# Optimization experiments

Measured on AMD Instinct MI355X. Metric: run time of the kernel, lower is better.

Reference implementation:

```python
import jax, jax.numpy as jnp
import numpy as np

NEG_POS = 3  # negpos_ratio from init
NEG_IOU = 0.4  # hard-coded in the torch forward


def corner_form(boxes):
    # (cx, cy, w, h) -> (x1, y1, x2, y2)
    cxcy, wh = boxes[:, :2], boxes[:, 2:]
    return jnp.concatenate([cxcy - wh / 2, cxcy + wh / 2], axis=-1)


def jaccard(a, b):
    # a: [O,4] corner boxes, b: [M,4] corner boxes -> IoU [O,M]
    lt = jnp.maximum(a[:, None, :2], b[None, :, :2])
    rb = jnp.minimum(a[:, None, 2:], b[None, :, 2:])
    wh = jnp.clip(rb - lt, 0.0, None)
    inter = wh[..., 0] * wh[..., 1]
    area_a = (a[:, 2] - a[:, 0]) * (a[:, 3] - a[:, 1])
    area_b = (b[:, 2] - b[:, 0]) * (b[:, 3] - b[:, 1])
    return inter / (area_a[:, None] + area_b[None, :] - inter)


def smooth_l1_sum(diff):
    ad = jnp.abs(diff)
    return jnp.where(ad < 1.0, 0.5 * diff * diff, ad - 0.5).sum()


def setup_inputs() -> dict:
    key = jax.random.key(0)
    k1, k2, k3, k4, k5, k6 = jax.random.split(key, 6)
    B, A, O = 32, 65536, 24
    loc_pred = jax.random.normal(k1, (B, A, 4), dtype=jnp.float32)
    conf_pred = jax.random.normal(k2, (B, A, 2), dtype=jnp.float32)
    # anchors in center form (cx, cy, w, h), all positive sizes
    cxcy = jax.random.uniform(k3, (A, 2), minval=0.0, maxval=1.0)
    wh = jax.random.uniform(k4, (A, 2), minval=0.02, maxval=0.3)
    anchors = jnp.concatenate([cxcy, wh], axis=-1).astype(jnp.float32)
    # GT: corner-form boxes with positive area, label column = 0 (binary head)
    xy1 = jax.random.uniform(k5, (B, O, 2), minval=0.0, maxval=0.7)
    gwh = jax.random.uniform(k6, (B, O, 2), minval=0.05, maxval=0.3)
    xy2 = jnp.clip(xy1 + gwh, 0.0, 1.0)
    labels = jnp.zeros((B, O, 1), dtype=jnp.float32)
    targets = jnp.concatenate([xy1, xy2, labels], axis=-1).astype(jnp.float32)
    return {"loc_pred": loc_pred, "conf_pred": conf_pred, "anchors": anchors,
            "targets": targets}


def reference(loc_pred, conf_pred, anchors, targets):
    B, A, _ = loc_pred.shape
    O = targets.shape[1]
    K = NEG_POS * O  # static top-k count (num_pos = O per image)
    anchors_c = jax.lax.stop_gradient(corner_form(anchors))

    def per_image(loc_p, conf_p, tgt):
        gt_boxes = tgt[:, :4]                       # [O,4]
        gt_labels = tgt[:, 4].astype(jnp.int32)     # [O]
        ov = jaccard(jax.lax.stop_gradient(gt_boxes), anchors_c)  # [O,A]
        match_idxs = jnp.argmax(ov, axis=1)         # best anchor per GT [O]
        iou = jnp.max(ov, axis=0)                   # best GT per anchor [A]
        loc_l = smooth_l1_sum(loc_p[match_idxs] - gt_boxes)
        pos = conf_p[match_idxs]                    # [O,2]
        # hard negative mining: among anchors with iou<0.4, take top K by
        # class-0 logit (descending sort + slice in the torch code)
        neg_scores = jnp.where(iou < NEG_IOU, conf_p[:, 0], -jnp.inf)
        _, neg_idx = jax.lax.top_k(neg_scores, K)
        neg = conf_p[neg_idx]                       # [K,2]
        logits = jnp.concatenate([pos, neg], axis=0)       # [O+K,2]
        labels = jnp.concatenate([gt_labels + 1,
                                  jnp.zeros((K,), jnp.int32)])
        ls = jax.nn.log_softmax(logits, axis=-1)
        ce = -ls[jnp.arange(O + K), labels].mean()
        return loc_l, ce

    loc_l, ce = jax.vmap(per_image)(loc_pred, conf_pred, targets)
    N = B * O  # sum of len(target) over batch
    return loc_l.sum() / N, ce.sum() / N
```

## Files before the change

### kernel.cpp

```cpp
#include <hip/hip_runtime.h>
#include <hip/hip_bf16.h>
#include <math.h>

typedef unsigned long long ull;

#define MAXO 24

__device__ __forceinline__ unsigned int xform(float x){
  unsigned int b = __float_as_uint(x);
  return (b & 0x80000000u) ? ~b : (b | 0x80000000u);
}
__device__ __forceinline__ float softplus_(float d){
  return (d > 20.f) ? d : log1pf(expf(d));
}

template<int O>
__global__ __launch_bounds__(256) void kA_t(const float4* __restrict__ anchors,
        const float* __restrict__ targets, const float2* __restrict__ conf,
        ull* __restrict__ matchbest, ull* __restrict__ negmask,
        unsigned int* __restrict__ gh1, int A){
  const int b = blockIdx.y, t = threadIdx.x, lane = t & 63;
  __shared__ ull wk[O][32];
  __shared__ unsigned int hist[2048];
  for (int i = t; i < 2048; i += 256) hist[i] = 0;
  __syncthreads();
  const float* tg = targets + (size_t)b * O * 5;
  const int base = blockIdx.x * 1024 + t;

  float ax1[4], ay1[4], ax2[4], ay2[4], aar[4], amax[4];
#pragma unroll
  for (int k = 0; k < 4; k++){
    float4 an = anchors[base + k*256];
    float hw = __fmul_rn(an.z, 0.5f), hh = __fmul_rn(an.w, 0.5f);
    ax1[k] = __fsub_rn(an.x, hw); ay1[k] = __fsub_rn(an.y, hh);
    ax2[k] = __fadd_rn(an.x, hw); ay2[k] = __fadd_rn(an.y, hh);
    aar[k] = __fmul_rn(__fsub_rn(ax2[k],ax1[k]), __fsub_rn(ay2[k],ay1[k]));
    amax[k] = 0.f;
  }

  unsigned int biou[O], bidx[O];
#pragma unroll
  for (int o = 0; o < O; o++){
    float gx1 = tg[o*5+0], gy1 = tg[o*5+1], gx2 = tg[o*5+2], gy2 = tg[o*5+3];
    float ga  = __fmul_rn(__fsub_rn(gx2,gx1), __fsub_rn(gy2,gy1));
    unsigned int bu = 0u, bi = 0u;
#pragma unroll
    for (int k = 0; k < 4; k++){
      float ltx = fmaxf(gx1, ax1[k]), lty = fmaxf(gy1, ay1[k]);
      float rbx = fminf(gx2, ax2[k]), rby = fminf(gy2, ay2[k]);
      float wx = fmaxf(__fsub_rn(rbx,ltx), 0.f);
      float wy = fmaxf(__fsub_rn(rby,lty), 0.f);
      float inter = __fmul_rn(wx, wy);
      float denom = __fsub_rn(__fadd_rn(ga, aar[k]), inter);
      float iou = __fmul_rn(inter, __builtin_amdgcn_rcpf(denom));
      amax[k] = fmaxf(amax[k], iou);
      unsigned int ub = __float_as_uint(iou);
      bool better = ub > bu;
      bi = better ? (unsigned int)(base + k*256) : bi;
      bu = better ? ub : bu;
    }
    biou[o] = bu; bidx[o] = bi;
  }

#pragma unroll
  for (int k = 0; k < 4; k++){
    bool neg = amax[k] < 0.4f;
    ull m = __ballot(neg);
    if (lane == 0) negmask[(size_t)b*(A>>6) + ((unsigned)(base + k*256) >> 6)] = m;
    if (neg){
      float cx = conf[(size_t)b*A + (unsigned)(base + k*256)].x;
      atomicAdd(&hist[xform(cx) >> 21], 1u);
    }
  }

#pragma unroll
  for (int o = 0; o < O; o++){
    ull key = ((ull)biou[o] << 32) | (unsigned int)(~bidx[o]);
#pragma unroll
    for (int s = 4; s >= 1; s >>= 1){
      ull other = (ull)__shfl_down((long long)key, (unsigned)s, 8);
      if (other > key) key = other;
    }
    if ((lane & 7) == 0) wk[o][t >> 3] = key;
  }
  __syncthreads();
  if (t < O * 8){
    int o = t >> 3, part = t & 7;
    ull k = wk[o][part*4];
#pragma unroll
    for (int j = 1; j < 4; j++){ ull v = wk[o][part*4 + j]; if (v > k) k = v; }
#pragma unroll
    for (int s = 4; s >= 1; s >>= 1){
      ull other = (ull)__shfl_down((long long)k, (unsigned)s, 8);
      if (other > k) k = other;
    }
    if (part == 0) atomicMax(&matchbest[b*O + o], k);
  }
  for (int i = t; i < 2048; i += 256){
    unsigned int v = hist[i];
    if (v) atomicAdd(&gh1[b*2048 + i], v);
  }
}

__global__ __launch_bounds__(256) void kA_g(const float4* __restrict__ anchors,
        const float* __restrict__ targets,
        ull* __restrict__ matchbest, ull* __restrict__ negmask, int A, int O){
  int b = blockIdx.y, t = threadIdx.x, lane = t & 63, wid = t >> 6;
  __shared__ float sgt[MAXO*5];
  __shared__ float sarea[MAXO];
  __shared__ ull wk[4][MAXO];
  int n5 = O*5;
  if (t < n5) sgt[t] = targets[b*n5 + t];
  __syncthreads();
  if (t < O){
    float x1=sgt[t*5], y1=sgt[t*5+1], x2=sgt[t*5+2], y2=sgt[t*5+3];
    sarea[t] = __fmul_rn(__fsub_rn(x2,x1), __fsub_rn(y2,y1));
  }
  __syncthreads();
  ull key[MAXO];
  for (int o=0;o<O;o++) key[o]=0;
  int base = blockIdx.x * 1024;
  for (int k=0;k<4;k++){
    int a = base + k*256 + t;
    float4 an = anchors[a];
    float hw = __fmul_rn(an.z, 0.5f), hh = __fmul_rn(an.w, 0.5f);
    float ax1 = __fsub_rn(an.x, hw), ay1 = __fsub_rn(an.y, hh);
    float ax2 = __fadd_rn(an.x, hw), ay2 = __fadd_rn(an.y, hh);
    float aarea = __fmul_rn(__fsub_rn(ax2,ax1), __fsub_rn(ay2,ay1));
    float amax = 0.f;
    for (int o=0;o<O;o++){
      float ltx = fmaxf(sgt[o*5+0], ax1), lty = fmaxf(sgt[o*5+1], ay1);
      float rbx = fminf(sgt[o*5+2], ax2), rby = fminf(sgt[o*5+3], ay2);
      float wx = fmaxf(__fsub_rn(rbx,ltx), 0.f);
      float wy = fmaxf(__fsub_rn(rby,lty), 0.f);
      float inter = __fmul_rn(wx, wy);
      float denom = __fsub_rn(__fadd_rn(sarea[o], aarea), inter);
      float iou = __fdiv_rn(inter, denom);
      amax = fmaxf(amax, iou);
      ull kk = ((ull)__float_as_uint(iou) << 32) | (unsigned int)(~(unsigned int)a);
      if (kk > key[o]) key[o] = kk;
    }
    ull m = __ballot(amax < 0.4f);
    if (lane == 0) negmask[(size_t)b*(A>>6) + (a>>6)] = m;
  }
  for (int o=0;o<O;o++){
    ull k = key[o];
    for (int s=32; s>=1; s>>=1){
      unsigned int lo = __shfl_down((unsigned int)(k & 0xFFFFFFFFu), s);
      unsigned int hi = __shfl_down((unsigned int)(k >> 32), s);
      ull other = ((ull)hi<<32) | lo;
      if (other > k) k = other;
    }
    if (lane == 0) wk[wid][o] = k;
  }
  __syncthreads();
  if (t < O){
    ull k = wk[0][t];
    for (int w=1; w<4; w++){ ull v = wk[w][t]; if (v>k) k=v; }
    atomicMax(&matchbest[b*O + t], k);
  }
}

__global__ __launch_bounds__(256) void kH1(const float2* __restrict__ conf,
     const ull* __restrict__ negmask, unsigned int* __restrict__ gh1, int A){
  int b = blockIdx.x, seg = blockIdx.y, t = threadIdx.x, lane = t & 63;
  __shared__ unsigned int h[2048];
  for (int i = t; i < 2048; i += 256) h[i] = 0;
  __syncthreads();
  const float2* cb = conf + (size_t)b * A;
  const ull* mb = negmask + (size_t)b * (A >> 6);
  int base = seg * 8192;
  for (int j = 0; j < 32; j++){
    int a = base + j*256 + t;
    ull w = mb[a >> 6];
    if ((w >> lane) & 1ull){
      unsigned int u = xform(cb[a].x);
      atomicAdd(&h[u >> 21], 1u);
    }
  }
  __syncthreads();
  for (int i = t; i < 2048; i += 256){
    unsigned int v = h[i];
    if (v) atomicAdd(&gh1[b*2048 + i], v);
  }
}

__global__ __launch_bounds__(1024) void kM2(const float2* __restrict__ conf,
     const ull* __restrict__ negmask, const unsigned int* __restrict__ gh1,
     const ull* __restrict__ matchbest, const float* __restrict__ loc,
     const float* __restrict__ targets, float* __restrict__ out,
     int A, int O, int K, float lscale, float cscale){
  const int b = blockIdx.x, t = threadIdx.x, lane = t & 63, wid = t >> 6;
  __shared__ unsigned int s0[2048], s1[2048];
  __shared__ ull stash[2048];
  __shared__ ull sb[256];
  __shared__ unsigned int s_cnt, s_cnt2, s_b1, s_R, s_b2, s_R2;
  __shared__ float wsum[16];

  if (t < O){
    int i = b*O + t;
    ull key = matchbest[i];
    unsigned int idx = ~(unsigned int)(key & 0xFFFFFFFFull);
    const float* tg = targets + (size_t)i*5;
    const float* lp = loc + ((size_t)b*A + idx)*4;
    float ll = 0.f;
#pragma unroll
    for (int d=0; d<4; d++){
      float df = lp[d] - tg[d];
      float ad = fabsf(df);
      ll += (ad < 1.f) ? 0.5f*df*df : (ad - 0.5f);
    }
    float2 c = conf[(size_t)b*A + idx];
    float m = fmaxf(c.x, c.y);
    float lse = m + logf(expf(c.x - m) + expf(c.y - m));
    atomicAdd(&out[0], ll * lscale);
    atomicAdd(&out[1], (lse - c.y) * cscale);
  }
  if (t == 0){ s_cnt = 0; s_cnt2 = 0; }
  for (int i = t; i < 2048; i += 1024) s0[i] = gh1[b*2048 + i];
  __syncthreads();

  {
    unsigned int* src = s0; unsigned int* dst = s1;
    for (int d = 1; d < 2048; d <<= 1){
      for (int i = t; i < 2048; i += 1024){
        unsigned int v = src[i];
        if (i + d < 2048) v += src[i + d];
        dst[i] = v;
      }
      __syncthreads();
      unsigned int* tmp = src; src = dst; dst = tmp;
    }
    for (int i = t; i < 2048; i += 1024){
      unsigned int si = src[i];
      unsigned int sn = (i < 2047) ? src[i+1] : 0u;
      if (si >= (unsigned int)K && sn < (unsigned int)K){ s_b1 = (unsigned int)i; s_R = (unsigned int)K - sn; }
    }
  }
  __syncthreads();
  const unsigned int b1 = s_b1, R = s_R;
  for (int i = t; i < 2048; i += 1024) s0[i] = 0;
  __syncthreads();

  float ce = 0.f;
  const float2* cb = conf + (size_t)b * A;
  const ull* mb = negmask + (size_t)b * (A >> 6);
  const int iters = A >> 10;
  for (int j = 0; j < iters; j++){
    int a = (j << 10) + t;
    ull w = mb[a >> 6];
    if ((w >> (a & 63)) & 1ull){
      float2 c = cb[a];
      unsigned int u = xform(c.x);
      unsigned int bin = u >> 21;
      if (bin > b1){
        ce += softplus_(c.y - c.x);
      } else if (bin == b1){
        atomicAdd(&s0[(u >> 10) & 2047u], 1u);
        unsigned int p = atomicAdd(&s_cnt, 1u);
        if (p < 2048u) stash[p] = ((ull)u << 32) | (unsigned int)(~(unsigned int)a);
      }
    }
  }
  __syncthreads();

  {
    unsigned int* src = s0; unsigned int* dst = s1;
    for (int d = 1; d < 2048; d <<= 1){
      for (int i = t; i < 2048; i += 1024){
        unsigned int v = src[i];
        if (i + d < 2048) v += src[i + d];
        dst[i] = v;
      }
      __syncthreads();
      unsigned int* tmp = src; src = dst; dst = tmp;
    }
    for (int i = t; i < 2048; i += 1024){
      unsigned int si = src[i];
      unsigned int sn = (i < 2047) ? src[i+1] : 0u;
      if (si >= R && sn < R){ s_b2 = (unsigned int)i; s_R2 = R - sn; }
    }
  }
  __syncthreads();
  const unsigned int b2 = s_b2, R2 = s_R2;
  const unsigned int cnt = (s_cnt < 2048u) ? s_cnt : 2048u;
  const bool ovf = (s_cnt > 2048u);

  if (!ovf){
    for (unsigned int i = t; i < cnt; i += 1024){
      ull e = stash[i];
      unsigned int u = (unsigned int)(e >> 32);
      unsigned int sub = (u >> 10) & 2047u;
      if (sub > b2){
        unsigned int a = ~(unsigned int)(e & 0xFFFFFFFFull);
        float2 c = cb[a];
        ce += softplus_(c.y - c.x);
      } else if (sub == b2){
        unsigned int p = atomicAdd(&s_cnt2, 1u);
        if (p < 256u) sb[p] = e;
      }
    }
  } else {
    for (int j = 0; j < iters; j++){
      int a = (j << 10) + t;
      ull w = mb[a >> 6];
      if ((w >> (a & 63)) & 1ull){
        float2 c = cb[a];
        unsigned int u = xform(c.x);
        if ((u >> 21) == b1){
          unsigned int sub = (u >> 10) & 2047u;
          if (sub > b2){
            ce += softplus_(c.y - c.x);
          } else if (sub == b2){
            unsigned int p = atomicAdd(&s_cnt2, 1u);
            if (p < 256u) sb[p] = ((ull)u << 32) | (unsigned int)(~(unsigned int)a);
          }
        }
      }
    }
  }
  __syncthreads();

  const unsigned int cnt2 = (s_cnt2 < 256u) ? s_cnt2 : 256u;
  for (unsigned int i = t; i < cnt2; i += 1024){
    ull ki = sb[i];
    unsigned int rank = 0;
    for (unsigned int j = 0; j < cnt2; j++) rank += (sb[j] > ki) ? 1u : 0u;
    if (rank < R2){
      unsigned int a = ~(unsigned int)(ki & 0xFFFFFFFFull);
      float2 c = cb[a];
      ce += softplus_(c.y - c.x);
    }
  }

#pragma unroll
  for (int s = 32; s >= 1; s >>= 1) ce += __shfl_down(ce, s);
  if (lane == 0) wsum[wid] = ce;
  __syncthreads();
  if (t == 0){
    float tot = 0.f;
    for (int w2 = 0; w2 < 16; w2++) tot += wsum[w2];
    atomicAdd(&out[1], tot * cscale);
  }
}

extern "C" void kernel_launch(void* const* d_in, const int* in_sizes, int n_in,
                              void* d_out, int out_size, void* d_ws, size_t ws_size,
                              hipStream_t stream) {
  const float*  loc     = (const float*)d_in[0];
  const float2* conf    = (const float2*)d_in[1];
  const float4* anchors = (const float4*)d_in[2];
  const float*  targets = (const float*)d_in[3];
  int A = in_sizes[2] / 4;
  int B = in_sizes[0] / (A * 4);
  int O = in_sizes[3] / (B * 5);
  int K = 3 * O;
  float* out = (float*)d_out;

  char* wsb = (char*)d_ws;
  size_t off = 0;
  ull* matchbest = (ull*)(wsb + off);              off += (size_t)B * O * sizeof(ull);
  unsigned int* gh1 = (unsigned int*)(wsb + off);  off += (size_t)B * 2048 * 4;
  size_t zbytes = off;
  off = (off + 7) & ~(size_t)7;
  ull* negmask = (ull*)(wsb + off);                off += (size_t)B * (A >> 6) * sizeof(ull);

  hipMemsetAsync(d_ws, 0, zbytes, stream);
  hipMemsetAsync(d_out, 0, 2*sizeof(float), stream);

  float lscale = 1.0f / (float)(B*O);
  float cscale = 1.0f / ((float)(O+K) * (float)(B*O));

  dim3 gA(A/1024, B);
  if (O == 24){
    kA_t<24><<<gA, 256, 0, stream>>>(anchors, targets, conf, matchbest, negmask, gh1, A);
  } else {
    kA_g<<<gA, 256, 0, stream>>>(anchors, targets, matchbest, negmask, A, O);
    dim3 gS(B, A/8192);
    kH1<<<gS, 256, 0, stream>>>(conf, negmask, gh1, A);
  }
  kM2<<<B, 1024, 0, stream>>>(conf, negmask, gh1, matchbest, loc, targets, out,
                              A, O, K, lscale, cscale);
}
```

Before: 189.3 us.

## Split per-image top-k selection into threshold, wide scan, and finalize kernels

```diff
diff --git a/kernel.cpp b/kernel.cpp
--- a/kernel.cpp
+++ b/kernel.cpp
@@ -5,6 +5,7 @@
 typedef unsigned long long ull;
 
 #define MAXO 24
+#define GCAP 2048u
 
 __device__ __forceinline__ unsigned int xform(float x){
   unsigned int b = __float_as_uint(x);
@@ -185,18 +186,13 @@
   }
 }
 
-__global__ __launch_bounds__(1024) void kM2(const float2* __restrict__ conf,
-     const ull* __restrict__ negmask, const unsigned int* __restrict__ gh1,
-     const ull* __restrict__ matchbest, const float* __restrict__ loc,
-     const float* __restrict__ targets, float* __restrict__ out,
+__global__ __launch_bounds__(256) void kT1(const unsigned int* __restrict__ gh1,
+     unsigned int* __restrict__ thr, const ull* __restrict__ matchbest,
+     const float* __restrict__ loc, const float* __restrict__ targets,
+     const float2* __restrict__ conf, float* __restrict__ out,
      int A, int O, int K, float lscale, float cscale){
-  const int b = blockIdx.x, t = threadIdx.x, lane = t & 63, wid = t >> 6;
+  int b = blockIdx.x, t = threadIdx.x;
   __shared__ unsigned int s0[2048], s1[2048];
-  __shared__ ull stash[2048];
-  __shared__ ull sb[256];
-  __shared__ unsigned int s_cnt, s_cnt2, s_b1, s_R, s_b2, s_R2;
-  __shared__ float wsum[16];
-
   if (t < O){
     int i = b*O + t;
     ull key = matchbest[i];
@@ -216,14 +212,89 @@
     atomicAdd(&out[0], ll * lscale);
     atomicAdd(&out[1], (lse - c.y) * cscale);
   }
-  if (t == 0){ s_cnt = 0; s_cnt2 = 0; }
-  for (int i = t; i < 2048; i += 1024) s0[i] = gh1[b*2048 + i];
-  __syncthreads();
-
+  for (int i = t; i < 2048; i += 256) s0[i] = gh1[b*2048 + i];
+  __syncthreads();
+  unsigned int* src = s0; unsigned int* dst = s1;
+  for (int d = 1; d < 2048; d <<= 1){
+    for (int i = t; i < 2048; i += 256){
+      unsigned int v = src[i];
+      if (i + d < 2048) v += src[i + d];
+      dst[i] = v;
+    }
+    __syncthreads();
+    unsigned int* tmp = src; src = dst; dst = tmp;
+  }
+  for (int i = t; i < 2048; i += 256){
+    unsigned int si = src[i];
+    unsigned int sn = (i < 2047) ? src[i+1] : 0u;
+    if (si >= (unsigned int)K && sn < (unsigned int)K){
+      thr[b*2]   = (unsigned int)i;
+      thr[b*2+1] = (unsigned int)K - sn;
+    }
+  }
+}
+
+__global__ __launch_bounds__(256) void kW(const float2* __restrict__ conf,
+     const ull* __restrict__ negmask, const unsigned int* __restrict__ thr,
+     unsigned int* __restrict__ gh2, unsigned int* __restrict__ gcnt,
+     ull* __restrict__ glist, float* __restrict__ out, int A, float cscale){
+  const int b = blockIdx.x, seg = blockIdx.y, t = threadIdx.x;
+  const int lane = t & 63, wid = t >> 6;
+  __shared__ unsigned int h2[2048];
+  __shared__ float wsum[4];
+  for (int i = t; i < 2048; i += 256) h2[i] = 0;
+  __syncthreads();
+  const unsigned int b1 = thr[b*2];
+  const float2* cb = conf + (size_t)b * A;
+  const ull* mb = negmask + (size_t)b * (A >> 6);
+  const int base = seg * 2048;
+  float ce = 0.f;
+#pragma unroll
+  for (int j = 0; j < 8; j++){
+    int a = base + j*256 + t;
+    ull w = mb[a >> 6];
+    if ((w >> lane) & 1ull){
+      float2 c = cb[a];
+      unsigned int u = xform(c.x);
+      unsigned int bin = u >> 21;
+      if (bin > b1){
+        ce += softplus_(c.y - c.x);
+      } else if (bin == b1){
+        atomicAdd(&h2[(u >> 10) & 2047u], 1u);
+        unsigned int p = atomicAdd(&gcnt[b], 1u);
+        if (p < GCAP) glist[(size_t)b*GCAP + p] = ((ull)u << 32) | (unsigned int)(~(unsigned int)a);
+      }
+    }
+  }
+#pragma unroll
+  for (int s = 32; s >= 1; s >>= 1) ce += __shfl_down(ce, s);
+  if (lane == 0) wsum[wid] = ce;
+  __syncthreads();
+  if (t == 0) atomicAdd(&out[1], (wsum[0]+wsum[1]+wsum[2]+wsum[3]) * cscale);
+  for (int i = t; i < 2048; i += 256){
+    unsigned int v = h2[i];
+    if (v) atomicAdd(&gh2[b*2048 + i], v);
+  }
+}
+
+__global__ __launch_bounds__(256) void kF2(const float2* __restrict__ conf,
+     const ull* __restrict__ negmask, const unsigned int* __restrict__ thr,
+     const unsigned int* __restrict__ gh2, const unsigned int* __restrict__ gcnt,
+     const ull* __restrict__ glist, float* __restrict__ out, int A, float cscale){
+  const int b = blockIdx.x, t = threadIdx.x, lane = t & 63, wid = t >> 6;
+  __shared__ unsigned int s0[2048], s1[2048];
+  __shared__ ull sb[256];
+  __shared__ unsigned int s_b2, s_R2, s_cnt2;
+  __shared__ float wsum[4];
+  const unsigned int b1 = thr[b*2];
+  const unsigned int R  = thr[b*2+1];
+  if (t == 0){ s_b2 = 0; s_R2 = R; s_cnt2 = 0; }
+  for (int i = t; i < 2048; i += 256) s0[i] = gh2[b*2048 + i];
+  __syncthreads();
   {
     unsigned int* src = s0; unsigned int* dst = s1;
     for (int d = 1; d < 2048; d <<= 1){
-      for (int i = t; i < 2048; i += 1024){
+      for (int i = t; i < 2048; i += 256){
         unsigned int v = src[i];
         if (i + d < 2048) v += src[i + d];
         dst[i] = v;
@@ -231,51 +302,7 @@
       __syncthreads();
       unsigned int* tmp = src; src = dst; dst = tmp;
     }
-    for (int i = t; i < 2048; i += 1024){
-      unsigned int si = src[i];
-      unsigned int sn = (i < 2047) ? src[i+1] : 0u;
-      if (si >= (unsigned int)K && sn < (unsigned int)K){ s_b1 = (unsigned int)i; s_R = (unsigned int)K - sn; }
-    }
-  }
-  __syncthreads();
-  const unsigned int b1 = s_b1, R = s_R;
-  for (int i = t; i < 2048; i += 1024) s0[i] = 0;
-  __syncthreads();
-
-  float ce = 0.f;
-  const float2* cb = conf + (size_t)b * A;
-  const ull* mb = negmask + (size_t)b * (A >> 6);
-  const int iters = A >> 10;
-  for (int j = 0; j < iters; j++){
-    int a = (j << 10) + t;
-    ull w = mb[a >> 6];
-    if ((w >> (a & 63)) & 1ull){
-      float2 c = cb[a];
-      unsigned int u = xform(c.x);
-      unsigned int bin = u >> 21;
-      if (bin > b1){
-        ce += softplus_(c.y - c.x);
-      } else if (bin == b1){
-        atomicAdd(&s0[(u >> 10) & 2047u], 1u);
-        unsigned int p = atomicAdd(&s_cnt, 1u);
-        if (p < 2048u) stash[p] = ((ull)u << 32) | (unsigned int)(~(unsigned int)a);
-      }
-    }
-  }
-  __syncthreads();
-
-  {
-    unsigned int* src = s0; unsigned int* dst = s1;
-    for (int d = 1; d < 2048; d <<= 1){
-      for (int i = t; i < 2048; i += 1024){
-        unsigned int v = src[i];
-        if (i + d < 2048) v += src[i + d];
-        dst[i] = v;
-      }
-      __syncthreads();
-      unsigned int* tmp = src; src = dst; dst = tmp;
-    }
-    for (int i = t; i < 2048; i += 1024){
+    for (int i = t; i < 2048; i += 256){
       unsigned int si = src[i];
       unsigned int sn = (i < 2047) ? src[i+1] : 0u;
       if (si >= R && sn < R){ s_b2 = (unsigned int)i; s_R2 = R - sn; }
@@ -283,12 +310,15 @@
   }
   __syncthreads();
   const unsigned int b2 = s_b2, R2 = s_R2;
-  const unsigned int cnt = (s_cnt < 2048u) ? s_cnt : 2048u;
-  const bool ovf = (s_cnt > 2048u);
+  const unsigned int rawcnt = gcnt[b];
+  const unsigned int cnt = (rawcnt < GCAP) ? rawcnt : GCAP;
+  const bool ovf = (rawcnt > GCAP);
+  const float2* cb = conf + (size_t)b * A;
+  float ce = 0.f;
 
   if (!ovf){
-    for (unsigned int i = t; i < cnt; i += 1024){
-      ull e = stash[i];
+    for (unsigned int i = t; i < cnt; i += 256){
+      ull e = glist[(size_t)b*GCAP + i];
       unsigned int u = (unsigned int)(e >> 32);
       unsigned int sub = (u >> 10) & 2047u;
       if (sub > b2){
@@ -301,8 +331,9 @@
       }
     }
   } else {
-    for (int j = 0; j < iters; j++){
-      int a = (j << 10) + t;
+    const ull* mb = negmask + (size_t)b * (A >> 6);
+    for (int j = 0; j < (A >> 8); j++){
+      int a = (j << 8) + t;
       ull w = mb[a >> 6];
       if ((w >> (a & 63)) & 1ull){
         float2 c = cb[a];
@@ -320,9 +351,8 @@
     }
   }
   __syncthreads();
-
   const unsigned int cnt2 = (s_cnt2 < 256u) ? s_cnt2 : 256u;
-  for (unsigned int i = t; i < cnt2; i += 1024){
+  for (unsigned int i = t; i < cnt2; i += 256){
     ull ki = sb[i];
     unsigned int rank = 0;
     for (unsigned int j = 0; j < cnt2; j++) rank += (sb[j] > ki) ? 1u : 0u;
@@ -332,16 +362,11 @@
       ce += softplus_(c.y - c.x);
     }
   }
-
 #pragma unroll
   for (int s = 32; s >= 1; s >>= 1) ce += __shfl_down(ce, s);
   if (lane == 0) wsum[wid] = ce;
   __syncthreads();
-  if (t == 0){
-    float tot = 0.f;
-    for (int w2 = 0; w2 < 16; w2++) tot += wsum[w2];
-    atomicAdd(&out[1], tot * cscale);
-  }
+  if (t == 0) atomicAdd(&out[1], (wsum[0]+wsum[1]+wsum[2]+wsum[3]) * cscale);
 }
 
 extern "C" void kernel_launch(void* const* d_in, const int* in_sizes, int n_in,
@@ -360,10 +385,14 @@
   char* wsb = (char*)d_ws;
   size_t off = 0;
   ull* matchbest = (ull*)(wsb + off);              off += (size_t)B * O * sizeof(ull);
-  unsigned int* gh1 = (unsigned int*)(wsb + off);  off += (size_t)B * 2048 * 4;
+  unsigned int* gh1  = (unsigned int*)(wsb + off); off += (size_t)B * 2048 * 4;
+  unsigned int* gh2  = (unsigned int*)(wsb + off); off += (size_t)B * 2048 * 4;
+  unsigned int* gcnt = (unsigned int*)(wsb + off); off += (size_t)B * 4;
+  unsigned int* thr  = (unsigned int*)(wsb + off); off += (size_t)B * 2 * 4;
   size_t zbytes = off;
   off = (off + 7) & ~(size_t)7;
   ull* negmask = (ull*)(wsb + off);                off += (size_t)B * (A >> 6) * sizeof(ull);
+  ull* glist   = (ull*)(wsb + off);                off += (size_t)B * GCAP * sizeof(ull);
 
   hipMemsetAsync(d_ws, 0, zbytes, stream);
   hipMemsetAsync(d_out, 0, 2*sizeof(float), stream);
@@ -379,6 +408,9 @@
     dim3 gS(B, A/8192);
     kH1<<<gS, 256, 0, stream>>>(conf, negmask, gh1, A);
   }
-  kM2<<<B, 1024, 0, stream>>>(conf, negmask, gh1, matchbest, loc, targets, out,
-                              A, O, K, lscale, cscale);
-}
+  kT1<<<B, 256, 0, stream>>>(gh1, thr, matchbest, loc, targets, conf, out,
+                             A, O, K, lscale, cscale);
+  dim3 gW(B, A/2048);
+  kW<<<gW, 256, 0, stream>>>(conf, negmask, thr, gh2, gcnt, glist, out, A, cscale);
+  kF2<<<B, 256, 0, stream>>>(conf, negmask, thr, gh2, gcnt, glist, out, A, cscale);
+}
```

Measured after the change: 174.7 us. 7.7% less time.
